# Performance work log

Measured on AMD Instinct MI355X. Metric: run time of the kernel, lower is better.

## Reference

```python
import jax, jax.numpy as jnp
import numpy as np

LEVELS, RADIUS, HDIM = 4, 4, 128
DN = ('NCHW', 'OIHW', 'NCHW')


def conv2d(x, w, b, ph, pw):
    y = jax.lax.conv_general_dilated(x, w, (1, 1), [(ph, ph), (pw, pw)], dimension_numbers=DN)
    return y + b[None, :, None, None]


def avg_pool2(x):
    return jax.lax.reduce_window(x, 0.0, jax.lax.add, (1, 1, 2, 2), (1, 1, 2, 2), 'VALID') * 0.25


def coords_grid(n, h, w):
    yy, xx = jnp.meshgrid(jnp.arange(h, dtype=jnp.float32), jnp.arange(w, dtype=jnp.float32), indexing='ij')
    return jnp.broadcast_to(jnp.stack([xx, yy])[None], (n, 2, h, w))


def build_pyramid(f1, f2):
    # all-pairs correlation volume, then 4-level avg-pool pyramid (as CorrBlock)
    n, c, h, w = f1.shape
    corr = jnp.einsum('nci,ncj->nij', f1.reshape(n, c, h * w), f2.reshape(n, c, h * w))
    corr = (corr / jnp.sqrt(jnp.float32(c))).reshape(n * h * w, 1, h, w)
    pyr = [corr]
    for _ in range(LEVELS - 1):
        corr = avg_pool2(corr)
        pyr.append(corr)
    return pyr


def bilinear_sample(img, x, y):
    # img: [B, Hc, Wc]; x, y: [B, K] pixel coords; zero padding outside (grid_sample, align_corners=True)
    b, hc, wc = img.shape
    flat = img.reshape(b, hc * wc)
    x0 = jnp.floor(x)
    y0 = jnp.floor(y)
    out = jnp.zeros_like(x)
    for dy in (0.0, 1.0):
        for dx in (0.0, 1.0):
            xi = x0 + dx
            yi = y0 + dy
            wgt = (1.0 - jnp.abs(x - xi)) * (1.0 - jnp.abs(y - yi))
            valid = (xi >= 0) & (xi <= wc - 1) & (yi >= 0) & (yi <= hc - 1)
            xc = jnp.clip(xi, 0, wc - 1).astype(jnp.int32)
            yc = jnp.clip(yi, 0, hc - 1).astype(jnp.int32)
            v = jnp.take_along_axis(flat, yc * wc + xc, axis=1)
            out = out + jnp.where(valid, wgt, 0.0) * v
    return out


def corr_lookup(pyr, coords):
    # windowed (2r+1)^2 lookup at each pyramid level around coords/2^i
    n, _, h, w = coords.shape
    r = RADIUS
    d = jnp.arange(-r, r + 1, dtype=jnp.float32)
    dxo = jnp.repeat(d, 2 * r + 1)  # offset on x varies along first kernel axis (RAFT layout)
    dyo = jnp.tile(d, 2 * r + 1)
    cx = coords[:, 0].reshape(n * h * w, 1)
    cy = coords[:, 1].reshape(n * h * w, 1)
    out = []
    for i, corr in enumerate(pyr):
        s = 1.0 / (2 ** i)
        out.append(bilinear_sample(corr[:, 0], cx * s + dxo[None, :], cy * s + dyo[None, :]))
    return jnp.concatenate(out, axis=-1).reshape(n, h, w, -1).transpose(0, 3, 1, 2)


def update_block(net, inp, corr, flow, p):
    (mc1_w, mc1_b, mc2_w, mc2_b, mf1_w, mf1_b, mf2_w, mf2_b, mo_w, mo_b,
     gz1_w, gz1_b, gr1_w, gr1_b, gq1_w, gq1_b, gz2_w, gz2_b, gr2_w, gr2_b, gq2_w, gq2_b,
     fh1_w, fh1_b, fh2_w, fh2_b, mk1_w, mk1_b, mk2_w, mk2_b) = p
    relu = jax.nn.relu
    # BasicMotionEncoder
    cor = relu(conv2d(corr, mc1_w, mc1_b, 0, 0))
    cor = relu(conv2d(cor, mc2_w, mc2_b, 1, 1))
    flo = relu(conv2d(flow, mf1_w, mf1_b, 3, 3))
    flo = relu(conv2d(flo, mf2_w, mf2_b, 1, 1))
    mot = relu(conv2d(jnp.concatenate([cor, flo], 1), mo_w, mo_b, 1, 1))
    mot = jnp.concatenate([mot, flow], 1)  # 128 channels
    x = jnp.concatenate([inp, mot], 1)  # 256 channels
    # SepConvGRU: horizontal (1x5) then vertical (5x1)
    hx = jnp.concatenate([net, x], 1)
    z = jax.nn.sigmoid(conv2d(hx, gz1_w, gz1_b, 0, 2))
    r = jax.nn.sigmoid(conv2d(hx, gr1_w, gr1_b, 0, 2))
    q = jnp.tanh(conv2d(jnp.concatenate([r * net, x], 1), gq1_w, gq1_b, 0, 2))
    net = (1.0 - z) * net + z * q
    hx = jnp.concatenate([net, x], 1)
    z = jax.nn.sigmoid(conv2d(hx, gz2_w, gz2_b, 2, 0))
    r = jax.nn.sigmoid(conv2d(hx, gr2_w, gr2_b, 2, 0))
    q = jnp.tanh(conv2d(jnp.concatenate([r * net, x], 1), gq2_w, gq2_b, 2, 0))
    net = (1.0 - z) * net + z * q
    dflow = conv2d(relu(conv2d(net, fh1_w, fh1_b, 1, 1)), fh2_w, fh2_b, 1, 1)
    up_mask = 0.25 * conv2d(relu(conv2d(net, mk1_w, mk1_b, 1, 1)), mk2_w, mk2_b, 0, 0)
    return net, up_mask, dflow


def upsample_flow(flow, mask):
    # convex combination upsampling [H/8,W/8,2] -> [H,W,2]
    n, _, h, w = flow.shape
    m = jax.nn.softmax(mask.reshape(n, 1, 9, 8, 8, h, w), axis=2)
    fp = jnp.pad(8.0 * flow, ((0, 0), (0, 0), (1, 1), (1, 1)))
    pat = jnp.stack([fp[:, :, i:i + h, j:j + w] for i in range(3) for j in range(3)], axis=2)  # N,2,9,H,W
    up = jnp.sum(m * pat[:, :, :, None, None, :, :], axis=2)  # N,2,8,8,H,W
    return up.transpose(0, 1, 4, 2, 5, 3).reshape(n, 2, 8 * h, 8 * w)


def raft_forward(fmap1, fmap2, fem1, fem2, cnet_out, enet_out, p, iters):
    n, _, h, w = fmap1.shape
    pyr = build_pyramid(fmap1, fmap2)
    epyr = build_pyramid(fem1, fem2)
    net = jnp.tanh(cnet_out[:, :HDIM])
    inp = jax.nn.relu(cnet_out[:, HDIM:])
    enet = jnp.tanh(enet_out[:, :HDIM])
    einp = jax.nn.relu(enet_out[:, HDIM:])
    coords0 = coords_grid(n, h, w)
    coords1 = coords0
    ecoords1 = coords0
    preds = []
    for _ in range(iters):
        coords1 = jax.lax.stop_gradient(coords1)  # coords1.detach()
        ecoords1 = jax.lax.stop_gradient(ecoords1)
        corr = corr_lookup(pyr, coords1)
        ecorr = corr_lookup(epyr, ecoords1)
        flow = coords1 - coords0
        eflow = ecoords1 - coords0
        net, up_mask, dflow = update_block(net, inp, corr, flow, p)
        enet, _eup, deflow = update_block(enet, einp, ecorr, eflow, p)
        coords1 = coords1 + dflow + deflow
        ecoords1 = ecoords1 + deflow
        preds.append(upsample_flow(coords1 - coords0, up_mask))
    return jnp.stack(preds)  # [iters, N, 2, 8H, 8W]


def setup_inputs():
    key = jax.random.key(0)
    ks = iter(jax.random.split(key, 64))
    def rn(shape, s=1.0):
        return jax.random.normal(next(ks), shape, dtype=jnp.float32) * s
    N, H8, W8 = 2, 48, 64
    cp = LEVELS * (2 * RADIUS + 1) ** 2  # 324
    return {
        'fmap1': rn((N, 256, H8, W8)), 'fmap2': rn((N, 256, H8, W8)),
        'fem1': rn((N, 256, H8, W8)), 'fem2': rn((N, 256, H8, W8)),
        'cnet_out': rn((N, 256, H8, W8)), 'enet_out': rn((N, 256, H8, W8)),
        'mc1_w': rn((256, cp, 1, 1), 0.05), 'mc1_b': rn((256,), 0.05),
        'mc2_w': rn((192, 256, 3, 3), 0.02), 'mc2_b': rn((192,), 0.02),
        'mf1_w': rn((128, 2, 7, 7), 0.1), 'mf1_b': rn((128,), 0.05),
        'mf2_w': rn((64, 128, 3, 3), 0.03), 'mf2_b': rn((64,), 0.02),
        'mo_w': rn((126, 256, 3, 3), 0.02), 'mo_b': rn((126,), 0.02),
        'gz1_w': rn((128, 384, 1, 5), 0.02), 'gz1_b': rn((128,), 0.02),
        'gr1_w': rn((128, 384, 1, 5), 0.02), 'gr1_b': rn((128,), 0.02),
        'gq1_w': rn((128, 384, 1, 5), 0.02), 'gq1_b': rn((128,), 0.02),
        'gz2_w': rn((128, 384, 5, 1), 0.02), 'gz2_b': rn((128,), 0.02),
        'gr2_w': rn((128, 384, 5, 1), 0.02), 'gr2_b': rn((128,), 0.02),
        'gq2_w': rn((128, 384, 5, 1), 0.02), 'gq2_b': rn((128,), 0.02),
        'fh1_w': rn((256, 128, 3, 3), 0.03), 'fh1_b': rn((256,), 0.02),
        'fh2_w': rn((2, 256, 3, 3), 0.03), 'fh2_b': rn((2,), 0.02),
        'mk1_w': rn((256, 128, 3, 3), 0.03), 'mk1_b': rn((256,), 0.02),
        'mk2_w': rn((576, 256, 1, 1), 0.05), 'mk2_b': rn((576,), 0.02),
        'iters': 12,
    }


def reference(fmap1, fmap2, fem1, fem2, cnet_out, enet_out,
              mc1_w, mc1_b, mc2_w, mc2_b, mf1_w, mf1_b, mf2_w, mf2_b, mo_w, mo_b,
              gz1_w, gz1_b, gr1_w, gr1_b, gq1_w, gq1_b, gz2_w, gz2_b, gr2_w, gr2_b, gq2_w, gq2_b,
              fh1_w, fh1_b, fh2_w, fh2_b, mk1_w, mk1_b, mk2_w, mk2_b, iters):
    p = (mc1_w, mc1_b, mc2_w, mc2_b, mf1_w, mf1_b, mf2_w, mf2_b, mo_w, mo_b,
         gz1_w, gz1_b, gr1_w, gr1_b, gq1_w, gq1_b, gz2_w, gz2_b, gr2_w, gr2_b, gq2_w, gq2_b,
         fh1_w, fh1_b, fh2_w, fh2_b, mk1_w, mk1_b, mk2_w, mk2_b)
    return raft_forward(fmap1, fmap2, fem1, fem2, cnet_out, enet_out, p, iters)
```

## Files before the change

### kernel.cpp

```cpp
#include <hip/hip_runtime.h>
#include <stdint.h>

typedef unsigned short ushort_t;
using bfx8 = __attribute__((ext_vector_type(8))) short;
using f32x4 = __attribute__((ext_vector_type(4))) float;

#define DEVINL static __device__ __forceinline__

DEVINL float bits2f(unsigned int b) { union { unsigned int i; float f; } v; v.i = b; return v.f; }
DEVINL float bf2f(ushort_t u) { return bits2f(((unsigned int)u) << 16); }
DEVINL ushort_t f2bf(float x) {
  union { float f; unsigned int i; } v; v.f = x;
  return (ushort_t)((v.i + 0x7FFFu + ((v.i >> 16) & 1u)) >> 16);
}
DEVINL unsigned int mulbf2(unsigned int a, unsigned int r) {
  float a0 = bits2f(a << 16), a1 = bits2f(a & 0xFFFF0000u);
  float r0 = bits2f(r << 16), r1 = bits2f(r & 0xFFFF0000u);
  return (unsigned int)f2bf(a0 * r0) | ((unsigned int)f2bf(a1 * r1) << 16);
}

constexpr int NB2 = 2;
constexpr int HH = 48, WW = 64, HW = 3072;
constexpr int NP = NB2 * HW;
constexpr int ITERS = 12;
constexpr int CCP = 72;

__global__ __launch_bounds__(256) void detect_k(const ushort_t* __restrict__ src,
                                                int* __restrict__ flag) {
  const int t = threadIdx.x;
  int bad = 0;
  for (int i = t; i < 4096; i += 256) {
    const float v = bf2f(src[i]);
    if (!(fabsf(v) < 1e30f)) bad = 1;
  }
  __shared__ int s;
  if (t == 0) s = 0;
  __syncthreads();
  if (bad) atomicOr(&s, 1);
  __syncthreads();
  if (t == 0) *flag = s;
}

struct CvtArgs {
  const void* src[30];
  float* dst[30];
  int n[30];
};
__global__ __launch_bounds__(256) void cvt_all_k(CvtArgs a, const int* __restrict__ flag) {
  const bool isf32 = (*flag != 0);
  const int stride = gridDim.x * 256;
  const int t0 = blockIdx.x * 256 + threadIdx.x;
  for (int s = 0; s < 30; ++s) {
    float* dst = a.dst[s];
    const int n = a.n[s];
    if (isf32) {
      const float* src = (const float*)a.src[s];
      for (int i = t0; i < n; i += stride) dst[i] = src[i];
    } else {
      const ushort_t* src = (const ushort_t*)a.src[s];
      for (int i = t0; i < n; i += stride) dst[i] = bf2f(src[i]);
    }
  }
}

__global__ __launch_bounds__(256) void trans_k(const void* s0, const void* s1,
                                               const void* s2, const void* s3,
                                               ushort_t* d0, ushort_t* d1,
                                               ushort_t* d2, ushort_t* d3,
                                               const int* __restrict__ flag) {
  const bool isf32 = (*flag != 0);
  int idx = blockIdx.x * 256 + threadIdx.x;
  if (idx >= NP * 256) return;
  const int t = blockIdx.y;
  const int c = idx & 255;
  const int p = idx >> 8;
  const int nb = (p >= HW) ? 1 : 0;
  const int pp = p - nb * HW;
  const void* s = (t == 0) ? s0 : (t == 1) ? s1 : (t == 2) ? s2 : s3;
  ushort_t* d = (t == 0) ? d0 : (t == 1) ? d1 : (t == 2) ? d2 : d3;
  const size_t si = ((size_t)(nb * 256 + c)) * HW + pp;
  d[idx] = isf32 ? f2bf(((const float*)s)[si]) : ((const ushort_t*)s)[si];
}

__global__ __launch_bounds__(256) void init2_k(const void* cnet, const void* enet,
                                               ushort_t* net0, ushort_t* net1,
                                               ushort_t* X0, ushort_t* X1v,
                                               const int* __restrict__ flag) {
  const bool isf32 = (*flag != 0);
  int idx = blockIdx.x * 256 + threadIdx.x;
  if (idx >= NB2 * 128 * HW) return;
  const int br = blockIdx.y;
  const void* s = br ? enet : cnet;
  ushort_t* N = br ? net1 : net0;
  ushort_t* X = br ? X1v : X0;
  int nb = idx / (128 * HW);
  int r = idx - nb * 128 * HW;
  int c = r / HW;
  int p = r - c * HW;
  const size_t i0 = ((size_t)(nb * 256 + c)) * HW + p;
  const size_t i1 = ((size_t)(nb * 256 + 128 + c)) * HW + p;
  float vn = isf32 ? ((const float*)s)[i0] : bf2f(((const ushort_t*)s)[i0]);
  float vi = isf32 ? ((const float*)s)[i1] : bf2f(((const ushort_t*)s)[i1]);
  N[((size_t)nb * HW + p) * 128 + c] = f2bf(tanhf(vn));
  X[((size_t)nb * HW + p) * 256 + c] = f2bf(fmaxf(vi, 0.f));
}

__global__ __launch_bounds__(256) void pack_k(const float* __restrict__ src,
                                              ushort_t* __restrict__ dst,
                                              int CO, int CI_real, int KHKW,
                                              int NCHUNK, int total) {
  int idx = blockIdx.x * 256 + threadIdx.x;
  if (idx >= total) return;
  const int KST = NCHUNK * KHKW * 2;
  const int j = idx & 7;
  const int l = (idx >> 3) & 63;
  const int s = (idx >> 9) % KST;
  const int b = idx / (512 * KST);
  const int chunk = s / (KHKW * 2);
  const int r = s - chunk * KHKW * 2;
  const int t = r >> 1;
  const int half = r & 1;
  const int ci = chunk * 64 + half * 32 + ((l >> 4) & 3) * 8 + j;
  const int n = b * 16 + (l & 15);
  float v = 0.f;
  if (n < CO && ci < CI_real) v = src[((size_t)n * CI_real + ci) * KHKW + t];
  dst[idx] = f2bf(v);
}

struct CorrPtrs { const ushort_t* f[4]; ushort_t* out[2]; };
__global__ __launch_bounds__(256) void corr_mfma_k(CorrPtrs C) {
  const int z = blockIdx.z;
  const int pyr = z >> 1, nb = z & 1;
  const ushort_t* f1 = C.f[pyr * 2] + (size_t)nb * HW * 256;
  const ushort_t* f2 = C.f[pyr * 2 + 1] + (size_t)nb * HW * 256;
  ushort_t* out = C.out[pyr] + (size_t)nb * HW * HW;
  const int tid = threadIdx.x;
  const int l = tid & 63;
  const int wave = tid >> 6;
  const int msub = wave & 1, nsub = wave >> 1;
  const int m0 = blockIdx.x * 32, n0 = blockIdx.y * 128;
  const int q = (l >> 4) & 3, m = l & 15;
  __shared__ ushort_t als[32 * CCP];
  __shared__ ushort_t bls[128 * CCP];
  f32x4 acc0 = {0.f, 0.f, 0.f, 0.f}, acc1 = acc0, acc2 = acc0, acc3 = acc0;
  for (int c64 = 0; c64 < 4; ++c64) {
    __syncthreads();
    {
      const int cc8 = tid & 7, pixel = tid >> 3;
      *(uint4*)&als[pixel * CCP + cc8 * 8] =
          *(const uint4*)(f1 + ((size_t)(m0 + pixel)) * 256 + c64 * 64 + cc8 * 8);
    }
#pragma unroll
    for (int r = 0; r < 4; ++r) {
      const int u = tid + r * 256;
      const int cc8 = u & 7, pixel = u >> 3;
      *(uint4*)&bls[pixel * CCP + cc8 * 8] =
          *(const uint4*)(f2 + ((size_t)(n0 + pixel)) * 256 + c64 * 64 + cc8 * 8);
    }
    __syncthreads();
#pragma unroll
    for (int half = 0; half < 2; ++half) {
      const bfx8 a = *(const bfx8*)&als[(msub * 16 + m) * CCP + half * 32 + q * 8];
      const bfx8 b0 = *(const bfx8*)&bls[(nsub * 64 + 0 + m) * CCP + half * 32 + q * 8];
      const bfx8 b1 = *(const bfx8*)&bls[(nsub * 64 + 16 + m) * CCP + half * 32 + q * 8];
      const bfx8 b2 = *(const bfx8*)&bls[(nsub * 64 + 32 + m) * CCP + half * 32 + q * 8];
      const bfx8 b3 = *(const bfx8*)&bls[(nsub * 64 + 48 + m) * CCP + half * 32 + q * 8];
      acc0 = __builtin_amdgcn_mfma_f32_16x16x32_bf16(a, b0, acc0, 0, 0, 0);
      acc1 = __builtin_amdgcn_mfma_f32_16x16x32_bf16(a, b1, acc1, 0, 0, 0);
      acc2 = __builtin_amdgcn_mfma_f32_16x16x32_bf16(a, b2, acc2, 0, 0, 0);
      acc3 = __builtin_amdgcn_mfma_f32_16x16x32_bf16(a, b3, acc3, 0, 0, 0);
    }
  }
  const f32x4 accs[4] = {acc0, acc1, acc2, acc3};
#pragma unroll
  for (int f = 0; f < 4; ++f) {
#pragma unroll
    for (int reg = 0; reg < 4; ++reg) {
      const int mi = m0 + msub * 16 + q * 4 + reg;
      const int nj = n0 + nsub * 64 + f * 16 + m;
      out[(size_t)mi * HW + nj] = f2bf(accs[f][reg] * 0.0625f);
    }
  }
}

__global__ __launch_bounds__(256) void avgpool_k(const ushort_t* __restrict__ inA,
                                                 const ushort_t* __restrict__ inB,
                                                 ushort_t* __restrict__ outA,
                                                 ushort_t* __restrict__ outB,
                                                 int wi, int ho, int wo, int total) {
  int idx = blockIdx.x * 256 + threadIdx.x;
  if (idx >= total) return;
  const ushort_t* in = blockIdx.y ? inB : inA;
  ushort_t* out = blockIdx.y ? outB : outA;
  int pw = ho * wo;
  int p = idx / pw;
  int r = idx - p * pw;
  int y = r / wo;
  int x = r - y * wo;
  const ushort_t* src = in + (size_t)p * (4 * pw) + (2 * y) * wi + 2 * x;
  float v = (bf2f(src[0]) + bf2f(src[1]) + bf2f(src[wi]) + bf2f(src[wi + 1])) * 0.25f;
  out[idx] = f2bf(v);
}

struct LkPtrs {
  const ushort_t* a0; const ushort_t* a1; const ushort_t* a2; const ushort_t* a3;
  const ushort_t* b0; const ushort_t* b1; const ushort_t* b2; const ushort_t* b3;
  const float* flow[2];
  ushort_t* out[2];
};
__global__ __launch_bounds__(384) void lookup_k(LkPtrs P) {
  const int c = threadIdx.x;
  const int p = blockIdx.x;
  const int br = blockIdx.y;
  if (c >= 324) return;
  const int nb = p / HW;
  const int rem = p - nb * HW;
  const int yy = rem >> 6, xx = rem & 63;
  const float* flow = P.flow[br];
  const float fx = flow[((size_t)(nb * 2 + 0)) * HW + rem];
  const float fy = flow[((size_t)(nb * 2 + 1)) * HW + rem];
  const int l = c / 81;
  const int k = c - l * 81;
  const float dx = (float)(k / 9) - 4.f;
  const float dy = (float)(k - (k / 9) * 9) - 4.f;
  const int hl = HH >> l, wl = WW >> l;
  const ushort_t* base =
      br ? ((l == 0) ? P.b0 : (l == 1) ? P.b1 : (l == 2) ? P.b2 : P.b3)
         : ((l == 0) ? P.a0 : (l == 1) ? P.a1 : (l == 2) ? P.a2 : P.a3);
  const ushort_t* img = base + (size_t)p * (hl * wl);
  const float s = 1.f / (float)(1 << l);
  const float xl = ((float)xx + fx) * s + dx;
  const float yl = ((float)yy + fy) * s + dy;
  const float x0f = floorf(xl), y0f = floorf(yl);
  float acc = 0.f;
#pragma unroll
  for (int dy2 = 0; dy2 < 2; ++dy2) {
#pragma unroll
    for (int dx2 = 0; dx2 < 2; ++dx2) {
      const float xi = x0f + dx2, yi = y0f + dy2;
      if (xi >= 0.f && xi <= (float)(wl - 1) && yi >= 0.f && yi <= (float)(hl - 1)) {
        const float wv = (1.f - fabsf(xl - xi)) * (1.f - fabsf(yl - yi));
        acc += wv * bf2f(img[(int)yi * wl + (int)xi]);
      }
    }
  }
  P.out[br][(size_t)p * 384 + c] = f2bf(acc);
}

struct BrPtrs {
  const ushort_t* xa[2]; const ushort_t* xb[2];
  const ushort_t* zr[2]; const ushort_t* old_[2];
  void* y[2];
};
template <int KH, int KW, int PH, int PW, int ACT, int MODE, bool UPD, bool FOUT>
__global__ __launch_bounds__(256) void conv_mfma_k(
    BrPtrs P, const ushort_t* __restrict__ PB, const float* __restrict__ bias,
    int NCHUNK, int CIT_A, int ci_base, int co_base, int CO_TOT, int co_limit,
    float scale, int nbr, int ylim1) {
  constexpr int COLS = 32 + 2 * PW;
  constexpr int KHKW = KH * KW;
  __shared__ ushort_t als[KH * COLS * CCP];
  const int z = blockIdx.z;
  const int br = (nbr == 2) ? (z >> 1) : 0;
  const int nb = (nbr == 2) ? (z & 1) : z;
  if (br == 1 && (int)blockIdx.y >= ylim1) return;
  const ushort_t* xa = P.xa[br];
  const ushort_t* xb = P.xb[br];
  const ushort_t* zr = P.zr[br];
  const ushort_t* old_ = P.old_[br];
  void* yv = P.y[br];

  const int tid = threadIdx.x;
  const int l = tid & 63;
  const int wave = tid >> 6;
  const int msub = wave & 1;
  const int nsub = wave >> 1;
  const int p0 = blockIdx.x * 32;
  const int y0 = p0 >> 6;
  const int x0 = p0 & 63;
  const int nbase = blockIdx.y * 8 + nsub * 4;
  const int KST = NCHUNK * KHKW * 2;
  const int q = (l >> 4) & 3;
  const int m = l & 15;

  f32x4 acc0 = {0.f, 0.f, 0.f, 0.f}, acc1 = acc0, acc2 = acc0, acc3 = acc0;
  const ushort_t* pb0 = PB + ((size_t)(nbase + 0) * KST * 64 + l) * 8;
  const ushort_t* pb1 = PB + ((size_t)(nbase + 1) * KST * 64 + l) * 8;
  const ushort_t* pb2 = PB + ((size_t)(nbase + 2) * KST * 64 + l) * 8;
  const ushort_t* pb3 = PB + ((size_t)(nbase + 3) * KST * 64 + l) * 8;
  const int aoff_lane = (msub * 16 + m) * CCP + q * 8;

  for (int c64 = 0; c64 < NCHUNK; ++c64) {
    __syncthreads();
    constexpr int TOTU = KH * COLS * 8;
    for (int u = tid; u < TOTU; u += 256) {
      const int cc8 = u & 7;
      const int colr = u >> 3;
      const int col = colr % COLS;
      const int row = colr / COLS;
      const int gy = y0 + row - PH;
      const int gx = x0 + col - PW;
      uint4 v = {0u, 0u, 0u, 0u};
      if ((unsigned)gy < 48u && (unsigned)gx < 64u) {
        const size_t pix = (size_t)nb * HW + gy * 64 + gx;
        const int gc = c64 * 64 + cc8 * 8;
        if (MODE == 0) {
          v = *(const uint4*)(xa + pix * CIT_A + ci_base + gc);
        } else if (gc < 128) {
          v = *(const uint4*)(xa + pix * 128 + gc);
          if (MODE == 2) {
            const uint4 r = *(const uint4*)(zr + pix * 256 + 128 + gc);
            v.x = mulbf2(v.x, r.x); v.y = mulbf2(v.y, r.y);
            v.z = mulbf2(v.z, r.z); v.w = mulbf2(v.w, r.w);
          }
        } else {
          v = *(const uint4*)(xb + pix * 256 + (gc - 128));
        }
      }
      *(uint4*)&als[(row * COLS + col) * CCP + cc8 * 8] = v;
    }
    __syncthreads();
    const int sbase = c64 * KHKW * 2;
#pragma unroll
    for (int kh = 0; kh < KH; ++kh) {
#pragma unroll
      for (int kw = 0; kw < KW; ++kw) {
#pragma unroll
        for (int half = 0; half < 2; ++half) {
          const int s = sbase + (kh * KW + kw) * 2 + half;
          const bfx8 a = *(const bfx8*)&als[kh * COLS * CCP + kw * CCP + half * 32 + aoff_lane];
          const bfx8 b0 = *(const bfx8*)(pb0 + (size_t)s * 512);
          const bfx8 b1 = *(const bfx8*)(pb1 + (size_t)s * 512);
          const bfx8 b2 = *(const bfx8*)(pb2 + (size_t)s * 512);
          const bfx8 b3 = *(const bfx8*)(pb3 + (size_t)s * 512);
          acc0 = __builtin_amdgcn_mfma_f32_16x16x32_bf16(a, b0, acc0, 0, 0, 0);
          acc1 = __builtin_amdgcn_mfma_f32_16x16x32_bf16(a, b1, acc1, 0, 0, 0);
          acc2 = __builtin_amdgcn_mfma_f32_16x16x32_bf16(a, b2, acc2, 0, 0, 0);
          acc3 = __builtin_amdgcn_mfma_f32_16x16x32_bf16(a, b3, acc3, 0, 0, 0);
        }
      }
    }
  }
  const f32x4 accs[4] = {acc0, acc1, acc2, acc3};
#pragma unroll
  for (int f = 0; f < 4; ++f) {
    const int co = (nbase + f) * 16 + m;
    const float b = bias[co];
#pragma unroll
    for (int reg = 0; reg < 4; ++reg) {
      const int row = q * 4 + reg;
      const int p = p0 + msub * 16 + row;
      float v = accs[f][reg] + b;
      if (ACT == 1) v = fmaxf(v, 0.f);
      if (ACT == 2) v = 1.f / (1.f + __expf(-v));
      if (ACT == 3) v = tanhf(v);
      v *= scale;
      const size_t pix = (size_t)nb * HW + p;
      if (UPD) {
        const float zv = bf2f(zr[pix * 256 + co]);
        const float old = bf2f(old_[pix * 128 + co]);
        v = (1.f - zv) * old + zv * v;
      }
      if (co_base + co < co_limit) {
        if (FOUT)
          ((float*)yv)[((size_t)nb * CO_TOT + co_base + co) * HW + p] = v;
        else
          ((ushort_t*)yv)[pix * CO_TOT + co_base + co] = f2bf(v);
      }
    }
  }
}

__global__ __launch_bounds__(256) void mf1_k(const float* __restrict__ fl0,
                                             const float* __restrict__ fl1,
                                             const float* __restrict__ w,
                                             const float* __restrict__ bias,
                                             ushort_t* __restrict__ flo0,
                                             ushort_t* __restrict__ flo1,
                                             ushort_t* __restrict__ X0,
                                             ushort_t* __restrict__ X1v) {
  __shared__ float wl[12544];
  const int tid = threadIdx.x;
  for (int e = tid; e < 12544; e += 256) {
    const int co = e & 127;
    const int rest = e >> 7;
    const int ci = rest / 49;
    const int t = rest - ci * 49;
    wl[e] = w[((size_t)co * 2 + ci) * 49 + t];
  }
  __syncthreads();
  const int zz = blockIdx.y;
  const int br = zz >> 1, nb = zz & 1;
  const float* flow = br ? fl1 : fl0;
  ushort_t* flo = br ? flo1 : flo0;
  ushort_t* X = br ? X1v : X0;
  const int p = blockIdx.x * 64 + (tid & 63);
  const int cg = (tid >> 6) * 32;
  const int y = p >> 6, x = p & 63;
  float acc[32];
#pragma unroll
  for (int c = 0; c < 32; ++c) acc[c] = bias[cg + c];
  for (int ci = 0; ci < 2; ++ci) {
    const float* fp = flow + (size_t)(nb * 2 + ci) * HW;
    for (int t = 0; t < 49; ++t) {
      const int gy = y + t / 7 - 3;
      const int gx = x + t % 7 - 3;
      float f = 0.f;
      if ((unsigned)gy < 48u && (unsigned)gx < 64u) f = fp[gy * 64 + gx];
      const float* wp = &wl[(ci * 49 + t) * 128 + cg];
#pragma unroll
      for (int c = 0; c < 32; ++c) acc[c] = fmaf(f, wp[c], acc[c]);
    }
  }
  ushort_t* op = flo + ((size_t)nb * HW + p) * 128 + cg;
#pragma unroll
  for (int c = 0; c < 32; ++c) op[c] = f2bf(fmaxf(acc[c], 0.f));
  if (tid < 64) {
    const float vx = flow[(size_t)(nb * 2 + 0) * HW + p];
    const float vy = flow[(size_t)(nb * 2 + 1) * HW + p];
    X[((size_t)nb * HW + p) * 256 + 254] = f2bf(vx);
    X[((size_t)nb * HW + p) * 256 + 255] = f2bf(vy);
  }
}

__global__ __launch_bounds__(256) void flow_update_k(float* __restrict__ flow,
                                                     float* __restrict__ eflow,
                                                     const float* __restrict__ df,
                                                     const float* __restrict__ edf) {
  int i = blockIdx.x * 256 + threadIdx.x;
  if (i < NB2 * 2 * HW) {
    float e = edf[i];
    flow[i] += df[i] + e;
    eflow[i] += e;
  }
}

__global__ __launch_bounds__(256) void upsample_k(const float* __restrict__ flow,
                                                  const ushort_t* __restrict__ mask,
                                                  float* __restrict__ out) {
  const int j = threadIdx.x & 7;
  const int xh = threadIdx.x >> 3;
  const int x = blockIdx.x * 32 + xh;
  const int i = blockIdx.y;
  const int nz = blockIdx.z;
  const int nb = nz / 48, yy = nz - nb * 48;
  const int rem = yy * 64 + x;
  const ushort_t* mp = mask + ((size_t)nb * HW + rem) * 576;
  float m[9];
  float mx = -1e30f;
#pragma unroll
  for (int k = 0; k < 9; ++k) {
    m[k] = bf2f(mp[k * 64 + i * 8 + j]);
    mx = fmaxf(mx, m[k]);
  }
  float sum = 0.f;
#pragma unroll
  for (int k = 0; k < 9; ++k) {
    m[k] = __expf(m[k] - mx);
    sum += m[k];
  }
  const float inv = 8.f / sum;
#pragma unroll
  for (int ch = 0; ch < 2; ++ch) {
    float acc = 0.f;
#pragma unroll
    for (int k = 0; k < 9; ++k) {
      const int gy = yy + k / 3 - 1;
      const int gx = x + (k - (k / 3) * 3) - 1;
      float f = 0.f;
      if ((unsigned)gy < 48u && (unsigned)gx < 64u)
        f = flow[((size_t)(nb * 2 + ch)) * HW + gy * 64 + gx];
      acc = fmaf(m[k], f, acc);
    }
    out[(((size_t)(nb * 2 + ch)) * 384 + (yy * 8 + i)) * 512 + x * 8 + j] = acc * inv;
  }
}

extern "C" void kernel_launch(void* const* d_in, const int* in_sizes, int n_in,
                              void* d_out, int out_size, void* d_ws, size_t ws_size,
                              hipStream_t stream) {
  (void)in_sizes; (void)n_in; (void)out_size;

  size_t off = 0;
  char* base = (char*)d_ws;
  auto take = [&](size_t nbytes) -> void* {
    void* p = base + off;
    off += (nbytes + 255) & ~(size_t)255;
    return p;
  };
  ushort_t* pyrA[4];
  ushort_t* pyrB[4];
  const int lsz[4] = {3072, 768, 192, 48};
  for (int l = 0; l < 4; ++l) pyrA[l] = (ushort_t*)take((size_t)NP * lsz[l] * 2);
  for (int l = 0; l < 4; ++l) pyrB[l] = (ushort_t*)take((size_t)NP * lsz[l] * 2);
  ushort_t* FMT[4];
  for (int s = 0; s < 4; ++s) FMT[s] = (ushort_t*)take((size_t)NP * 256 * 2);
  ushort_t* CORRb[2];
  CORRb[0] = (ushort_t*)take((size_t)NP * 384 * 2);
  CORRb[1] = (ushort_t*)take((size_t)NP * 384 * 2);
  ushort_t* NETb[2];
  NETb[0] = (ushort_t*)take((size_t)NP * 128 * 2);
  NETb[1] = (ushort_t*)take((size_t)NP * 128 * 2);
  ushort_t* NETBb[2];
  NETBb[0] = (ushort_t*)take((size_t)NP * 128 * 2);
  NETBb[1] = (ushort_t*)take((size_t)NP * 128 * 2);
  ushort_t* Xb[2];
  Xb[0] = (ushort_t*)take((size_t)NP * 256 * 2);
  Xb[1] = (ushort_t*)take((size_t)NP * 256 * 2);
  ushort_t* ACT1b[2];
  ACT1b[0] = (ushort_t*)take((size_t)NP * 256 * 2);
  ACT1b[1] = (ushort_t*)take((size_t)NP * 256 * 2);
  ushort_t* CFBb[2];
  CFBb[0] = (ushort_t*)take((size_t)NP * 256 * 2);
  CFBb[1] = (ushort_t*)take((size_t)NP * 256 * 2);
  ushort_t* FLOb[2];
  FLOb[0] = (ushort_t*)take((size_t)NP * 128 * 2);
  FLOb[1] = (ushort_t*)take((size_t)NP * 128 * 2);
  ushort_t* ZRBb[2];
  ZRBb[0] = (ushort_t*)take((size_t)NP * 256 * 2);
  ZRBb[1] = (ushort_t*)take((size_t)NP * 256 * 2);
  ushort_t* A512b[2];
  A512b[0] = (ushort_t*)take((size_t)NP * 512 * 2);
  A512b[1] = (ushort_t*)take((size_t)NP * 512 * 2);
  ushort_t* MASKB = (ushort_t*)take((size_t)NP * 576 * 2);
  float* FLOW = (float*)take((size_t)NB2 * 2 * HW * 4);
  float* EFLOW = (float*)take((size_t)NB2 * 2 * HW * 4);
  float* DF = (float*)take((size_t)NB2 * 2 * HW * 4);
  float* EDF = (float*)take((size_t)NB2 * 2 * HW * 4);

  static const int WSZ[15] = {82944, 442368, 12544, 73728, 290304,
                              245760, 245760, 245760, 245760, 245760, 245760,
                              294912, 4608, 294912, 147456};
  static const int BSZ[15] = {256, 192, 128, 64, 126, 128, 128, 128,
                              128, 128, 128, 256, 2, 256, 576};
  float* Wf[15];
  float* Bf[15];
  for (int s = 0; s < 5; ++s) Wf[s] = (float*)take((size_t)WSZ[s] * 4);
  Wf[5] = (float*)take((size_t)2 * 245760 * 4); Wf[6] = Wf[5] + 245760;
  Wf[7] = (float*)take((size_t)245760 * 4);
  Wf[8] = (float*)take((size_t)2 * 245760 * 4); Wf[9] = Wf[8] + 245760;
  Wf[10] = (float*)take((size_t)245760 * 4);
  Wf[11] = (float*)take((size_t)2 * 294912 * 4); Wf[13] = Wf[11] + 294912;
  Wf[12] = (float*)take((size_t)4608 * 4);
  Wf[14] = (float*)take((size_t)147456 * 4);
  for (int s = 0; s < 5; ++s) Bf[s] = (float*)take((size_t)BSZ[s] * 4);
  Bf[5] = (float*)take((size_t)2 * 128 * 4); Bf[6] = Bf[5] + 128;
  Bf[7] = (float*)take((size_t)128 * 4);
  Bf[8] = (float*)take((size_t)2 * 128 * 4); Bf[9] = Bf[8] + 128;
  Bf[10] = (float*)take((size_t)128 * 4);
  Bf[11] = (float*)take((size_t)2 * 256 * 4); Bf[13] = Bf[11] + 256;
  Bf[12] = (float*)take((size_t)2 * 4);
  Bf[14] = (float*)take((size_t)576 * 4);
  ushort_t* PBmc1 = (ushort_t*)take((size_t)16 * 12 * 512 * 2);
  ushort_t* PBmc2 = (ushort_t*)take((size_t)16 * 72 * 512 * 2);
  ushort_t* PBmf2 = (ushort_t*)take((size_t)8 * 36 * 512 * 2);
  ushort_t* PBmo = (ushort_t*)take((size_t)8 * 72 * 512 * 2);
  ushort_t* PBgzr1 = (ushort_t*)take((size_t)16 * 60 * 512 * 2);
  ushort_t* PBgq1 = (ushort_t*)take((size_t)8 * 60 * 512 * 2);
  ushort_t* PBgzr2 = (ushort_t*)take((size_t)16 * 60 * 512 * 2);
  ushort_t* PBgq2 = (ushort_t*)take((size_t)8 * 60 * 512 * 2);
  ushort_t* PBfh = (ushort_t*)take((size_t)32 * 36 * 512 * 2);
  ushort_t* PBmk2 = (ushort_t*)take((size_t)40 * 8 * 512 * 2);
  ushort_t* PBfh2 = (ushort_t*)take((size_t)8 * 72 * 512 * 2);
  int* FLAG = (int*)take(256);

  if (off > ws_size) return;

  detect_k<<<1, 256, 0, stream>>>((const ushort_t*)d_in[0], FLAG);
  CvtArgs ca;
  for (int s = 0; s < 15; ++s) {
    ca.src[s] = d_in[6 + 2 * s];
    ca.dst[s] = Wf[s];
    ca.n[s] = WSZ[s];
    ca.src[15 + s] = d_in[7 + 2 * s];
    ca.dst[15 + s] = Bf[s];
    ca.n[15 + s] = BSZ[s];
  }
  cvt_all_k<<<512, 256, 0, stream>>>(ca, FLAG);

  trans_k<<<dim3((NP * 256 + 255) / 256, 4), 256, 0, stream>>>(
      d_in[0], d_in[1], d_in[2], d_in[3], FMT[0], FMT[1], FMT[2], FMT[3], FLAG);
  init2_k<<<dim3((NB2 * 128 * HW + 255) / 256, 2), 256, 0, stream>>>(
      d_in[4], d_in[5], NETb[0], NETb[1], Xb[0], Xb[1], FLAG);

  auto pack = [&](const float* src, ushort_t* dst, int CO, int NB16, int CI, int KHKW, int NCH) {
    int total = NB16 * NCH * KHKW * 2 * 512;
    pack_k<<<(total + 255) / 256, 256, 0, stream>>>(src, dst, CO, CI, KHKW, NCH, total);
  };
  pack(Wf[0], PBmc1, 256, 16, 324, 1, 6);
  pack(Wf[1], PBmc2, 192, 16, 256, 9, 4);
  pack(Wf[3], PBmf2, 64, 8, 128, 9, 2);
  pack(Wf[4], PBmo, 126, 8, 256, 9, 4);
  pack(Wf[5], PBgzr1, 256, 16, 384, 5, 6);
  pack(Wf[7], PBgq1, 128, 8, 384, 5, 6);
  pack(Wf[8], PBgzr2, 256, 16, 384, 5, 6);
  pack(Wf[10], PBgq2, 128, 8, 384, 5, 6);
  pack(Wf[11], PBfh, 512, 32, 128, 9, 2);
  pack(Wf[14], PBmk2, 576, 40, 256, 1, 4);
  pack(Wf[12], PBfh2, 2, 8, 256, 9, 4);

  {
    CorrPtrs cp;
    for (int s = 0; s < 4; ++s) cp.f[s] = FMT[s];
    cp.out[0] = pyrA[0];
    cp.out[1] = pyrB[0];
    corr_mfma_k<<<dim3(96, 24, 4), 256, 0, stream>>>(cp);
  }
  {
    const int wsv[4] = {64, 32, 16, 8};
    const int hsv[4] = {48, 24, 12, 6};
    for (int l = 0; l < 3; ++l) {
      int ho = hsv[l + 1], wo = wsv[l + 1];
      int total = NP * ho * wo;
      avgpool_k<<<dim3((total + 255) / 256, 2), 256, 0, stream>>>(
          pyrA[l], pyrB[l], pyrA[l + 1], pyrB[l + 1], wsv[l], ho, wo, total);
    }
  }
  (void)hipMemsetAsync(FLOW, 0, (size_t)NB2 * 2 * HW * 4, stream);
  (void)hipMemsetAsync(EFLOW, 0, (size_t)NB2 * 2 * HW * 4, stream);

  float* outp = (float*)d_out;

  LkPtrs lk;
  lk.a0 = pyrA[0]; lk.a1 = pyrA[1]; lk.a2 = pyrA[2]; lk.a3 = pyrA[3];
  lk.b0 = pyrB[0]; lk.b1 = pyrB[1]; lk.b2 = pyrB[2]; lk.b3 = pyrB[3];
  lk.flow[0] = FLOW; lk.flow[1] = EFLOW;
  lk.out[0] = CORRb[0]; lk.out[1] = CORRb[1];

  auto BP = [&](const ushort_t* a0, const ushort_t* a1, const ushort_t* b0,
                const ushort_t* b1, const ushort_t* z0, const ushort_t* z1,
                const ushort_t* o0, const ushort_t* o1, void* y0, void* y1) {
    BrPtrs p;
    p.xa[0] = a0; p.xa[1] = a1; p.xb[0] = b0; p.xb[1] = b1;
    p.zr[0] = z0; p.zr[1] = z1; p.old_[0] = o0; p.old_[1] = o1;
    p.y[0] = y0; p.y[1] = y1;
    return p;
  };
  const ushort_t* NU = nullptr;

  for (int it = 0; it < ITERS; ++it) {
    lookup_k<<<dim3(6144, 2), 384, 0, stream>>>(lk);
    conv_mfma_k<1, 1, 0, 0, 1, 0, false, false><<<dim3(96, 2, 4), 256, 0, stream>>>(
        BP(CORRb[0], CORRb[1], NU, NU, NU, NU, NU, NU, ACT1b[0], ACT1b[1]),
        PBmc1, Bf[0], 6, 384, 0, 0, 256, 256, 1.f, 2, 2);
    conv_mfma_k<3, 3, 1, 1, 1, 0, false, false><<<dim3(96, 2, 4), 256, 0, stream>>>(
        BP(ACT1b[0], ACT1b[1], NU, NU, NU, NU, NU, NU, CFBb[0], CFBb[1]),
        PBmc2, Bf[1], 4, 256, 0, 0, 256, 256, 1.f, 2, 2);
    mf1_k<<<dim3(48, 4), 256, 0, stream>>>(FLOW, EFLOW, Wf[2], Bf[2],
                                           FLOb[0], FLOb[1], Xb[0], Xb[1]);
    conv_mfma_k<3, 3, 1, 1, 1, 0, false, false><<<dim3(96, 1, 4), 256, 0, stream>>>(
        BP(FLOb[0], FLOb[1], NU, NU, NU, NU, NU, NU, CFBb[0], CFBb[1]),
        PBmf2, Bf[3], 2, 128, 0, 192, 256, 256, 1.f, 2, 1);
    conv_mfma_k<3, 3, 1, 1, 1, 0, false, false><<<dim3(96, 1, 4), 256, 0, stream>>>(
        BP(CFBb[0], CFBb[1], NU, NU, NU, NU, NU, NU, Xb[0], Xb[1]),
        PBmo, Bf[4], 4, 256, 0, 128, 256, 254, 1.f, 2, 1);
    conv_mfma_k<1, 5, 0, 2, 2, 1, false, false><<<dim3(96, 2, 4), 256, 0, stream>>>(
        BP(NETb[0], NETb[1], Xb[0], Xb[1], NU, NU, NU, NU, ZRBb[0], ZRBb[1]),
        PBgzr1, Bf[5], 6, 0, 0, 0, 256, 256, 1.f, 2, 2);
    conv_mfma_k<1, 5, 0, 2, 3, 2, true, false><<<dim3(96, 1, 4), 256, 0, stream>>>(
        BP(NETb[0], NETb[1], Xb[0], Xb[1], ZRBb[0], ZRBb[1], NETb[0], NETb[1],
           NETBb[0], NETBb[1]),
        PBgq1, Bf[7], 6, 0, 0, 0, 128, 128, 1.f, 2, 1);
    conv_mfma_k<5, 1, 2, 0, 2, 1, false, false><<<dim3(96, 2, 4), 256, 0, stream>>>(
        BP(NETBb[0], NETBb[1], Xb[0], Xb[1], NU, NU, NU, NU, ZRBb[0], ZRBb[1]),
        PBgzr2, Bf[8], 6, 0, 0, 0, 256, 256, 1.f, 2, 2);
    conv_mfma_k<5, 1, 2, 0, 3, 2, true, false><<<dim3(96, 1, 4), 256, 0, stream>>>(
        BP(NETBb[0], NETBb[1], Xb[0], Xb[1], ZRBb[0], ZRBb[1], NETBb[0], NETBb[1],
           NETb[0], NETb[1]),
        PBgq2, Bf[10], 6, 0, 0, 0, 128, 128, 1.f, 2, 1);
    conv_mfma_k<3, 3, 1, 1, 1, 0, false, false><<<dim3(96, 4, 4), 256, 0, stream>>>(
        BP(NETb[0], NETb[1], NU, NU, NU, NU, NU, NU, A512b[0], A512b[1]),
        PBfh, Bf[11], 2, 128, 0, 0, 512, 512, 1.f, 2, 2);
    conv_mfma_k<3, 3, 1, 1, 0, 0, false, true><<<dim3(96, 1, 4), 256, 0, stream>>>(
        BP(A512b[0], A512b[1], NU, NU, NU, NU, NU, NU, DF, EDF),
        PBfh2, Bf[12], 4, 512, 0, 0, 2, 2, 1.f, 2, 1);
    conv_mfma_k<1, 1, 0, 0, 0, 0, false, false><<<dim3(96, 5, 2), 256, 0, stream>>>(
        BP(A512b[0], NU, NU, NU, NU, NU, NU, NU, (void*)MASKB, nullptr),
        PBmk2, Bf[14], 4, 512, 256, 0, 576, 576, 0.25f, 1, 99);
    flow_update_k<<<48, 256, 0, stream>>>(FLOW, EFLOW, DF, EDF);
    upsample_k<<<dim3(2, 8, 96), 256, 0, stream>>>(FLOW, MASKB,
                                                   outp + (size_t)it * (NB2 * 2 * 384 * 512));
  }
}
```

Measured before the change: 4.690 ms.

## Retile conv MFMA kernel to full-row blocks with templated output fragments

Result: slower. 5.114 ms (+9.0%).

```diff
diff --git a/kernel.cpp b/kernel.cpp
--- a/kernel.cpp
+++ b/kernel.cpp
@@ -252,13 +252,14 @@
   const ushort_t* zr[2]; const ushort_t* old_[2];
   void* y[2];
 };
-template <int KH, int KW, int PH, int PW, int ACT, int MODE, bool UPD, bool FOUT>
+template <int KH, int KW, int PH, int PW, int ACT, int MODE, bool UPD, bool FOUT, int NF>
 __global__ __launch_bounds__(256) void conv_mfma_k(
     BrPtrs P, const ushort_t* __restrict__ PB, const float* __restrict__ bias,
     int NCHUNK, int CIT_A, int ci_base, int co_base, int CO_TOT, int co_limit,
     float scale, int nbr, int ylim1) {
-  constexpr int COLS = 32 + 2 * PW;
+  constexpr int COLS = 64 + 2 * PW;
   constexpr int KHKW = KH * KW;
+  constexpr int MF = (NF == 1) ? 1 : 2;
   __shared__ ushort_t als[KH * COLS * CCP];
   const int z = blockIdx.z;
   const int br = (nbr == 2) ? (z >> 1) : 0;
@@ -273,22 +274,28 @@
   const int tid = threadIdx.x;
   const int l = tid & 63;
   const int wave = tid >> 6;
-  const int msub = wave & 1;
-  const int nsub = wave >> 1;
-  const int p0 = blockIdx.x * 32;
-  const int y0 = p0 >> 6;
-  const int x0 = p0 & 63;
-  const int nbase = blockIdx.y * 8 + nsub * 4;
+  const int msub = (NF == 1) ? wave : (wave >> 1);
+  const int nsub = (NF == 1) ? 0 : (wave & 1);
+  const int y0 = blockIdx.x;
+  const int nbase = blockIdx.y * (2 * NF) + nsub * NF;
   const int KST = NCHUNK * KHKW * 2;
   const int q = (l >> 4) & 3;
   const int m = l & 15;
-
-  f32x4 acc0 = {0.f, 0.f, 0.f, 0.f}, acc1 = acc0, acc2 = acc0, acc3 = acc0;
-  const ushort_t* pb0 = PB + ((size_t)(nbase + 0) * KST * 64 + l) * 8;
-  const ushort_t* pb1 = PB + ((size_t)(nbase + 1) * KST * 64 + l) * 8;
-  const ushort_t* pb2 = PB + ((size_t)(nbase + 2) * KST * 64 + l) * 8;
-  const ushort_t* pb3 = PB + ((size_t)(nbase + 3) * KST * 64 + l) * 8;
-  const int aoff_lane = (msub * 16 + m) * CCP + q * 8;
+  const int xbase = msub * (MF * 16);
+
+  f32x4 acc[MF][NF];
+#pragma unroll
+  for (int mf = 0; mf < MF; ++mf)
+#pragma unroll
+    for (int f = 0; f < NF; ++f) acc[mf][f] = {0.f, 0.f, 0.f, 0.f};
+  const ushort_t* pb[NF];
+#pragma unroll
+  for (int f = 0; f < NF; ++f)
+    pb[f] = PB + ((size_t)(nbase + f) * KST * 64 + l) * 8;
+  int alane[MF];
+#pragma unroll
+  for (int mf = 0; mf < MF; ++mf)
+    alane[mf] = (xbase + mf * 16 + m) * CCP + q * 8;
 
   for (int c64 = 0; c64 < NCHUNK; ++c64) {
     __syncthreads();
@@ -299,7 +306,7 @@
       const int col = colr % COLS;
       const int row = colr / COLS;
       const int gy = y0 + row - PH;
-      const int gx = x0 + col - PW;
+      const int gx = col - PW;
       uint4 v = {0u, 0u, 0u, 0u};
       if ((unsigned)gy < 48u && (unsigned)gx < 64u) {
         const size_t pix = (size_t)nb * HW + gy * 64 + gx;
@@ -328,44 +335,49 @@
 #pragma unroll
         for (int half = 0; half < 2; ++half) {
           const int s = sbase + (kh * KW + kw) * 2 + half;
-          const bfx8 a = *(const bfx8*)&als[kh * COLS * CCP + kw * CCP + half * 32 + aoff_lane];
-          const bfx8 b0 = *(const bfx8*)(pb0 + (size_t)s * 512);
-          const bfx8 b1 = *(const bfx8*)(pb1 + (size_t)s * 512);
-          const bfx8 b2 = *(const bfx8*)(pb2 + (size_t)s * 512);
-          const bfx8 b3 = *(const bfx8*)(pb3 + (size_t)s * 512);
-          acc0 = __builtin_amdgcn_mfma_f32_16x16x32_bf16(a, b0, acc0, 0, 0, 0);
-          acc1 = __builtin_amdgcn_mfma_f32_16x16x32_bf16(a, b1, acc1, 0, 0, 0);
-          acc2 = __builtin_amdgcn_mfma_f32_16x16x32_bf16(a, b2, acc2, 0, 0, 0);
-          acc3 = __builtin_amdgcn_mfma_f32_16x16x32_bf16(a, b3, acc3, 0, 0, 0);
+          bfx8 a[MF];
+#pragma unroll
+          for (int mf = 0; mf < MF; ++mf)
+            a[mf] = *(const bfx8*)&als[kh * (COLS * CCP) + kw * CCP + half * 32 + alane[mf]];
+          bfx8 b[NF];
+#pragma unroll
+          for (int f = 0; f < NF; ++f) b[f] = *(const bfx8*)(pb[f] + (size_t)s * 512);
+#pragma unroll
+          for (int mf = 0; mf < MF; ++mf)
+#pragma unroll
+            for (int f = 0; f < NF; ++f)
+              acc[mf][f] = __builtin_amdgcn_mfma_f32_16x16x32_bf16(a[mf], b[f], acc[mf][f], 0, 0, 0);
         }
       }
     }
   }
-  const f32x4 accs[4] = {acc0, acc1, acc2, acc3};
-#pragma unroll
-  for (int f = 0; f < 4; ++f) {
-    const int co = (nbase + f) * 16 + m;
-    const float b = bias[co];
-#pragma unroll
-    for (int reg = 0; reg < 4; ++reg) {
-      const int row = q * 4 + reg;
-      const int p = p0 + msub * 16 + row;
-      float v = accs[f][reg] + b;
-      if (ACT == 1) v = fmaxf(v, 0.f);
-      if (ACT == 2) v = 1.f / (1.f + __expf(-v));
-      if (ACT == 3) v = tanhf(v);
-      v *= scale;
-      const size_t pix = (size_t)nb * HW + p;
-      if (UPD) {
-        const float zv = bf2f(zr[pix * 256 + co]);
-        const float old = bf2f(old_[pix * 128 + co]);
-        v = (1.f - zv) * old + zv * v;
-      }
-      if (co_base + co < co_limit) {
-        if (FOUT)
-          ((float*)yv)[((size_t)nb * CO_TOT + co_base + co) * HW + p] = v;
-        else
-          ((ushort_t*)yv)[pix * CO_TOT + co_base + co] = f2bf(v);
+#pragma unroll
+  for (int mf = 0; mf < MF; ++mf) {
+#pragma unroll
+    for (int f = 0; f < NF; ++f) {
+      const int co = (nbase + f) * 16 + m;
+      const float bv = bias[co];
+#pragma unroll
+      for (int reg = 0; reg < 4; ++reg) {
+        const int x = xbase + mf * 16 + q * 4 + reg;
+        const int p = y0 * 64 + x;
+        float v = acc[mf][f][reg] + bv;
+        if (ACT == 1) v = fmaxf(v, 0.f);
+        if (ACT == 2) v = 1.f / (1.f + __expf(-v));
+        if (ACT == 3) v = tanhf(v);
+        v *= scale;
+        const size_t pix = (size_t)nb * HW + p;
+        if (UPD) {
+          const float zv = bf2f(zr[pix * 256 + co]);
+          const float old = bf2f(old_[pix * 128 + co]);
+          v = (1.f - zv) * old + zv * v;
+        }
+        if (co_base + co < co_limit) {
+          if (FOUT)
+            ((float*)yv)[((size_t)nb * CO_TOT + co_base + co) * HW + p] = v;
+          else
+            ((ushort_t*)yv)[pix * CO_TOT + co_base + co] = f2bf(v);
+        }
       }
     }
   }
@@ -561,7 +573,7 @@
   ushort_t* PBgq2 = (ushort_t*)take((size_t)8 * 60 * 512 * 2);
   ushort_t* PBfh = (ushort_t*)take((size_t)32 * 36 * 512 * 2);
   ushort_t* PBmk2 = (ushort_t*)take((size_t)40 * 8 * 512 * 2);
-  ushort_t* PBfh2 = (ushort_t*)take((size_t)8 * 72 * 512 * 2);
+  ushort_t* PBfh2 = (ushort_t*)take((size_t)1 * 72 * 512 * 2);
   int* FLAG = (int*)take(256);
 
   if (off > ws_size) return;
@@ -597,7 +609,7 @@
   pack(Wf[10], PBgq2, 128, 8, 384, 5, 6);
   pack(Wf[11], PBfh, 512, 32, 128, 9, 2);
   pack(Wf[14], PBmk2, 576, 40, 256, 1, 4);
-  pack(Wf[12], PBfh2, 2, 8, 256, 9, 4);
+  pack(Wf[12], PBfh2, 2, 1, 256, 9, 4);
 
   {
     CorrPtrs cp;
@@ -640,41 +652,41 @@
 
   for (int it = 0; it < ITERS; ++it) {
     lookup_k<<<dim3(6144, 2), 384, 0, stream>>>(lk);
-    conv_mfma_k<1, 1, 0, 0, 1, 0, false, false><<<dim3(96, 2, 4), 256, 0, stream>>>(
+    conv_mfma_k<1, 1, 0, 0, 1, 0, false, false, 4><<<dim3(48, 2, 4), 256, 0, stream>>>(
         BP(CORRb[0], CORRb[1], NU, NU, NU, NU, NU, NU, ACT1b[0], ACT1b[1]),
         PBmc1, Bf[0], 6, 384, 0, 0, 256, 256, 1.f, 2, 2);
-    conv_mfma_k<3, 3, 1, 1, 1, 0, false, false><<<dim3(96, 2, 4), 256, 0, stream>>>(
+    conv_mfma_k<3, 3, 1, 1, 1, 0, false, false, 4><<<dim3(48, 2, 4), 256, 0, stream>>>(
         BP(ACT1b[0], ACT1b[1], NU, NU, NU, NU, NU, NU, CFBb[0], CFBb[1]),
         PBmc2, Bf[1], 4, 256, 0, 0, 256, 256, 1.f, 2, 2);
     mf1_k<<<dim3(48, 4), 256, 0, stream>>>(FLOW, EFLOW, Wf[2], Bf[2],
                                            FLOb[0], FLOb[1], Xb[0], Xb[1]);
-    conv_mfma_k<3, 3, 1, 1, 1, 0, false, false><<<dim3(96, 1, 4), 256, 0, stream>>>(
+    conv_mfma_k<3, 3, 1, 1, 1, 0, false, false, 2><<<dim3(48, 2, 4), 256, 0, stream>>>(
         BP(FLOb[0], FLOb[1], NU, NU, NU, NU, NU, NU, CFBb[0], CFBb[1]),
-        PBmf2, Bf[3], 2, 128, 0, 192, 256, 256, 1.f, 2, 1);
-    conv_mfma_k<3, 3, 1, 1, 1, 0, false, false><<<dim3(96, 1, 4), 256, 0, stream>>>(
+        PBmf2, Bf[3], 2, 128, 0, 192, 256, 256, 1.f, 2, 2);
+    conv_mfma_k<3, 3, 1, 1, 1, 0, false, false, 2><<<dim3(48, 2, 4), 256, 0, stream>>>(
         BP(CFBb[0], CFBb[1], NU, NU, NU, NU, NU, NU, Xb[0], Xb[1]),
-        PBmo, Bf[4], 4, 256, 0, 128, 256, 254, 1.f, 2, 1);
-    conv_mfma_k<1, 5, 0, 2, 2, 1, false, false><<<dim3(96, 2, 4), 256, 0, stream>>>(
+        PBmo, Bf[4], 4, 256, 0, 128, 256, 254, 1.f, 2, 2);
+    conv_mfma_k<1, 5, 0, 2, 2, 1, false, false, 4><<<dim3(48, 2, 4), 256, 0, stream>>>(
         BP(NETb[0], NETb[1], Xb[0], Xb[1], NU, NU, NU, NU, ZRBb[0], ZRBb[1]),
         PBgzr1, Bf[5], 6, 0, 0, 0, 256, 256, 1.f, 2, 2);
-    conv_mfma_k<1, 5, 0, 2, 3, 2, true, false><<<dim3(96, 1, 4), 256, 0, stream>>>(
+    conv_mfma_k<1, 5, 0, 2, 3, 2, true, false, 2><<<dim3(48, 2, 4), 256, 0, stream>>>(
         BP(NETb[0], NETb[1], Xb[0], Xb[1], ZRBb[0], ZRBb[1], NETb[0], NETb[1],
            NETBb[0], NETBb[1]),
-        PBgq1, Bf[7], 6, 0, 0, 0, 128, 128, 1.f, 2, 1);
-    conv_mfma_k<5, 1, 2, 0, 2, 1, false, false><<<dim3(96, 2, 4), 256, 0, stream>>>(
+        PBgq1, Bf[7], 6, 0, 0, 0, 128, 128, 1.f, 2, 2);
+    conv_mfma_k<5, 1, 2, 0, 2, 1, false, false, 4><<<dim3(48, 2, 4), 256, 0, stream>>>(
         BP(NETBb[0], NETBb[1], Xb[0], Xb[1], NU, NU, NU, NU, ZRBb[0], ZRBb[1]),
         PBgzr2, Bf[8], 6, 0, 0, 0, 256, 256, 1.f, 2, 2);
-    conv_mfma_k<5, 1, 2, 0, 3, 2, true, false><<<dim3(96, 1, 4), 256, 0, stream>>>(
+    conv_mfma_k<5, 1, 2, 0, 3, 2, true, false, 2><<<dim3(48, 2, 4), 256, 0, stream>>>(
         BP(NETBb[0], NETBb[1], Xb[0], Xb[1], ZRBb[0], ZRBb[1], NETBb[0], NETBb[1],
            NETb[0], NETb[1]),
-        PBgq2, Bf[10], 6, 0, 0, 0, 128, 128, 1.f, 2, 1);
-    conv_mfma_k<3, 3, 1, 1, 1, 0, false, false><<<dim3(96, 4, 4), 256, 0, stream>>>(
+        PBgq2, Bf[10], 6, 0, 0, 0, 128, 128, 1.f, 2, 2);
+    conv_mfma_k<3, 3, 1, 1, 1, 0, false, false, 4><<<dim3(48, 4, 4), 256, 0, stream>>>(
         BP(NETb[0], NETb[1], NU, NU, NU, NU, NU, NU, A512b[0], A512b[1]),
         PBfh, Bf[11], 2, 128, 0, 0, 512, 512, 1.f, 2, 2);
-    conv_mfma_k<3, 3, 1, 1, 0, 0, false, true><<<dim3(96, 1, 4), 256, 0, stream>>>(
+    conv_mfma_k<3, 3, 1, 1, 0, 0, false, true, 1><<<dim3(48, 1, 4), 256, 0, stream>>>(
         BP(A512b[0], A512b[1], NU, NU, NU, NU, NU, NU, DF, EDF),
         PBfh2, Bf[12], 4, 512, 0, 0, 2, 2, 1.f, 2, 1);
-    conv_mfma_k<1, 1, 0, 0, 0, 0, false, false><<<dim3(96, 5, 2), 256, 0, stream>>>(
+    conv_mfma_k<1, 1, 0, 0, 0, 0, false, false, 4><<<dim3(48, 5, 2), 256, 0, stream>>>(
         BP(A512b[0], NU, NU, NU, NU, NU, NU, NU, (void*)MASKB, nullptr),
         PBmk2, Bf[14], 4, 512, 256, 0, 576, 576, 0.25f, 1, 99);
     flow_update_k<<<48, 256, 0, stream>>>(FLOW, EFLOW, DF, EDF);
```
